# Kernel tuning notes

Measured on AMD Instinct MI355X. Metric: run time of the kernel, lower is better.

## Reference

```python
import jax, jax.numpy as jnp
import numpy as np

B, S, D, H = 8, 1024, 1024, 16
HD = D // H  # head dim 64
NUM_REL = 7


def setup_inputs() -> dict:
    key = jax.random.key(0)
    ks = jax.random.split(key, 10)
    s = 0.02
    return {
        "hidden_states": jax.random.normal(ks[0], (B, S, D), dtype=jnp.float32),
        "attention_mask": jnp.zeros((B, 1, 1, S), dtype=jnp.float32),
        "relation": jax.random.randint(ks[1], (B, S, S), 0, NUM_REL, dtype=jnp.int32),
        "Wq": jax.random.normal(ks[2], (D, D), dtype=jnp.float32) * s,
        "bq": jnp.zeros((D,), dtype=jnp.float32),
        "Wk": jax.random.normal(ks[3], (D, D), dtype=jnp.float32) * s,
        "bk": jnp.zeros((D,), dtype=jnp.float32),
        "Wv": jax.random.normal(ks[4], (D, D), dtype=jnp.float32) * s,
        "bv": jnp.zeros((D,), dtype=jnp.float32),
        "rel_emb": jax.random.normal(ks[5], (NUM_REL, H), dtype=jnp.float32) * s,
    }


def reference(hidden_states, attention_mask, relation, Wq, bq, Wk, bk, Wv, bv, rel_emb):
    def heads(x):  # [B,S,D] -> [B,H,S,HD]
        return x.reshape(B, S, H, HD).transpose(0, 2, 1, 3)

    q = heads(hidden_states @ Wq.T + bq)
    k = heads(hidden_states @ Wk.T + bk)
    v = heads(hidden_states @ Wv.T + bv)

    scores = jnp.einsum("bhqd,bhkd->bhqk", q, k) / jnp.sqrt(jnp.float32(HD))
    # relation bias: gather [B,S,S,H] then move H to dim 1
    rel_bias = rel_emb[relation].transpose(0, 3, 1, 2)  # [B,H,S,S]
    scores = scores + rel_bias + attention_mask
    probs = jax.nn.softmax(scores, axis=-1)  # dropout is identity in eval
    ctx = jnp.einsum("bhqk,bhkd->bhqd", probs, v)
    return ctx.transpose(0, 2, 1, 3).reshape(B, S, D)
```

## Files before the change

### kernel.cpp

```cpp
#include <hip/hip_runtime.h>

#define NB 8
#define NS 1024
#define ND 1024
#define NH 16
#define NHD 64

typedef __attribute__((ext_vector_type(8))) short bf16x8;
typedef __attribute__((ext_vector_type(4))) float f32x4;
typedef __attribute__((ext_vector_type(4))) unsigned int u32x4;

#define GLOAD_LDS16(g, l) __builtin_amdgcn_global_load_lds(                    \
    (const __attribute__((address_space(1))) void*)(g),                        \
    (__attribute__((address_space(3))) void*)(l), 16, 0, 0)

static __device__ __forceinline__ unsigned short f2bf(float f) {
    unsigned int u = __builtin_bit_cast(unsigned int, f);
    unsigned int r = u + 0x7fffu + ((u >> 16) & 1u);
    return (unsigned short)(r >> 16);
}

static __device__ __forceinline__ unsigned int cvtpk(float lo, float hi) {
    unsigned int r;
    asm("v_cvt_pk_bf16_f32 %0, %1, %2" : "=v"(r) : "v"(lo), "v"(hi));
    return r;
}

__global__ void cvt_f32_bf16(const float* __restrict__ in, unsigned short* __restrict__ out, int n) {
    int i = (blockIdx.x * blockDim.x + threadIdx.x) * 4;
    if (i >= n) return;
    float4 v = *reinterpret_cast<const float4*>(in + i);
    ushort4 o;
    o.x = f2bf(v.x); o.y = f2bf(v.y); o.z = f2bf(v.z); o.w = f2bf(v.w);
    *reinterpret_cast<ushort4*>(out + i) = o;
}

__global__ void cvt_w3(const float* __restrict__ Wq, const float* __restrict__ Wk,
                       const float* __restrict__ Wv, unsigned short* __restrict__ out) {
    const float* src = (blockIdx.y == 0) ? Wq : (blockIdx.y == 1) ? Wk : Wv;
    int i = (blockIdx.x * blockDim.x + threadIdx.x) * 4;
    float4 v = *reinterpret_cast<const float4*>(src + i);
    ushort4 o;
    o.x = f2bf(v.x); o.y = f2bf(v.y); o.z = f2bf(v.z); o.w = f2bf(v.w);
    *reinterpret_cast<ushort4*>(out + (size_t)blockIdx.y * (ND * ND) + i) = o;
}

__global__ void pack_rel8(const int* __restrict__ rel, unsigned int* __restrict__ out) {
    int i = blockIdx.x * blockDim.x + threadIdx.x;
    int4 v = reinterpret_cast<const int4*>(rel)[i];
    out[i] = (unsigned)v.x | ((unsigned)v.y << 8) | ((unsigned)v.z << 16) | ((unsigned)v.w << 24);
}

__global__ __launch_bounds__(256) void qkv_gemm(
    const unsigned short* __restrict__ A,
    const unsigned short* __restrict__ Wq, const unsigned short* __restrict__ Wk,
    const unsigned short* __restrict__ Wv,
    const float* __restrict__ bq, const float* __restrict__ bk, const float* __restrict__ bv,
    const float* __restrict__ mask,
    unsigned short* __restrict__ Qo, unsigned short* __restrict__ Ko, unsigned short* __restrict__ Vo)
{
    const int z = blockIdx.z;
    const unsigned short* W = (z == 0) ? Wq : (z == 1) ? Wk : Wv;
    const float* bias = (z == 0) ? bq : (z == 1) ? bk : bv;
    const int m0 = blockIdx.x * 128;
    const int n0 = blockIdx.y * 128;
    const float LOG2E = 1.4426950408889634f;

    __shared__ unsigned short As[128][64];
    __shared__ unsigned short Bs[128][64];

    const int tid = threadIdx.x;
    const int lane = tid & 63;
    const int wave = tid >> 6;
    const int wm = wave >> 1, wn = wave & 1;

    f32x4 acc[4][4] = {};

    const int crow = lane >> 3;
    const int gcol = ((lane & 7) ^ crow) * 8;
    const int kofs = (lane >> 4) * 8;

    for (int kb = 0; kb < ND; kb += 64) {
#pragma unroll
        for (int cc = 0; cc < 4; ++cc) {
            int c = wave * 4 + cc;
            GLOAD_LDS16(&A[(size_t)(m0 + c * 8 + crow) * ND + kb + gcol], &As[c * 8][0]);
            GLOAD_LDS16(&W[(size_t)(n0 + c * 8 + crow) * ND + kb + gcol], &Bs[c * 8][0]);
        }
        __syncthreads();
#pragma unroll
        for (int kk = 0; kk < 2; ++kk) {
            const int colx = (kk * 32 + kofs) ^ ((lane & 7) * 8);
            bf16x8 af[4], bfr[4];
#pragma unroll
            for (int i = 0; i < 4; ++i) {
                af[i]  = *reinterpret_cast<const bf16x8*>(&As[wm * 64 + i * 16 + (lane & 15)][colx]);
                bfr[i] = *reinterpret_cast<const bf16x8*>(&Bs[wn * 64 + i * 16 + (lane & 15)][colx]);
            }
#pragma unroll
            for (int mi = 0; mi < 4; ++mi)
#pragma unroll
                for (int ni = 0; ni < 4; ++ni)
                    acc[mi][ni] = __builtin_amdgcn_mfma_f32_16x16x32_bf16(af[mi], bfr[ni], acc[mi][ni], 0, 0, 0);
        }
        __syncthreads();
    }

#pragma unroll
    for (int ni = 0; ni < 4; ++ni) {
        int n = n0 + wn * 64 + ni * 16 + (lane & 15);
        float bv_ = bias[n];
        int h = n >> 6, hd = n & 63;
#pragma unroll
        for (int mi = 0; mi < 4; ++mi) {
            int m = m0 + wm * 64 + mi * 16 + (lane >> 4) * 4;
            int b = m >> 10, s = m & 1023;
            if (z == 2) {
                float4 mv = *reinterpret_cast<const float4*>(&mask[(size_t)b * NS + s]);
                ushort4 o;
                o.x = f2bf((acc[mi][ni][0] + bv_) * exp2f(mv.x * LOG2E));
                o.y = f2bf((acc[mi][ni][1] + bv_) * exp2f(mv.y * LOG2E));
                o.z = f2bf((acc[mi][ni][2] + bv_) * exp2f(mv.z * LOG2E));
                o.w = f2bf((acc[mi][ni][3] + bv_) * exp2f(mv.w * LOG2E));
                *reinterpret_cast<ushort4*>(&Vo[(((size_t)b * NH + h) * NHD + hd) * NS + s]) = o;
            } else {
                unsigned short* O = (z == 0) ? Qo : Ko;
#pragma unroll
                for (int r2 = 0; r2 < 4; ++r2)
                    O[(((size_t)b * NH + h) * NS + s + r2) * NHD + hd] = f2bf(acc[mi][ni][r2] + bv_);
            }
        }
    }
}

__global__ __launch_bounds__(512) void flash_attn(
    const unsigned short* __restrict__ Q, const unsigned short* __restrict__ Kb,
    const unsigned short* __restrict__ Vt,
    const unsigned char* __restrict__ rel8, const float* __restrict__ rel_emb,
    const float* __restrict__ mask, float* __restrict__ out)
{
    const int q0 = blockIdx.x * 128;
    const int h = blockIdx.y;
    const int b = blockIdx.z;
    const int tid = threadIdx.x, lane = tid & 63, wave = tid >> 6;
    const int g = lane >> 4, l15 = lane & 15;

    __shared__ unsigned short Ks[2][64][64];
    __shared__ unsigned short Vs[2][64][64];
    __shared__ unsigned short s_emask[NS];
    __shared__ float s_re2[8];
    const float LOG2E = 1.4426950408889634f;
    const float SCL2 = 0.125f * 1.4426950408889634f;
    if (tid < 7) s_re2[tid] = rel_emb[tid * NH + h] * LOG2E - 4.0f;

    const unsigned short* Qh = Q  + (((size_t)b * NH + h) * NS) * NHD;
    const unsigned short* Kh = Kb + (((size_t)b * NH + h) * NS) * NHD;
    const unsigned short* Vh = Vt + (((size_t)b * NH + h) * NHD) * NS;
    const int qg = q0 + wave * 16 + l15;
    const unsigned char* __restrict__ relrow = rel8 + (size_t)b * NS * NS + (size_t)qg * NS;
    const float* __restrict__ maskb = mask + (size_t)b * NS;

    bf16x8 qa[2];
    qa[0] = *reinterpret_cast<const bf16x8*>(&Qh[(size_t)qg * NHD + g * 8]);
    qa[1] = *reinterpret_cast<const bf16x8*>(&Qh[(size_t)qg * NHD + 32 + g * 8]);

    f32x4 ctx[4] = {};
    f32x4 l_acc = {};
    float mofs = 0.f;
    bool everscaled = false;

    const int crow = lane >> 3;
    const int gcol = ((lane & 7) ^ crow) * 8;
    const int swz8 = (lane & 7) * 8;

    const int rho = wave * 8 + crow;
    const int kvperm = ((rho >> 5) << 5) + (((rho >> 2) & 3) << 3)
                     + (((rho >> 4) & 1) << 2) + (rho & 3);

#define STAGE(buf, kv)                                                                          \
    {                                                                                           \
        GLOAD_LDS16(&Kh[(size_t)((kv) + kvperm) * NHD + gcol], &Ks[buf][wave * 8][0]);          \
        GLOAD_LDS16(&Vh[(size_t)(wave * 8 + crow) * NS + (kv) + gcol], &Vs[buf][wave * 8][0]);  \
    }

#define LOADRM(S, t0)                                                                \
    {                                                                                \
        r##S##a = *reinterpret_cast<const uint2*>(&relrow[(t0) * 64 + 8 * g]);       \
        r##S##b = *reinterpret_cast<const uint2*>(&relrow[(t0) * 64 + 32 + 8 * g]);  \
    }

    uint2 rAa, rAb, rBa, rBb;

    STAGE(0, 0)
    LOADRM(A, 0)
    s_emask[tid] = f2bf(exp2f(maskb[tid] * LOG2E));
    s_emask[tid + 512] = f2bf(exp2f(maskb[tid + 512] * LOG2E));
    __syncthreads();

#define BODY(cur, S, SN, tc, tn)                                               \
  {                                                                            \
    if ((tn) < 16) {                                                           \
      STAGE(cur ^ 1, (tn) * 64)                                                \
      LOADRM(SN, tn)                                                           \
    }                                                                          \
    f32x4 sc[4] = {};                                                          \
    __builtin_amdgcn_s_setprio(1);                                             \
    _Pragma("unroll")                                                          \
    for (int kk = 0; kk < 2; ++kk) {                                           \
      const int colx = (kk * 32 + g * 8) ^ swz8;                               \
      _Pragma("unroll")                                                        \
      for (int tt = 0; tt < 4; ++tt) {                                         \
        bf16x8 kfrag = *reinterpret_cast<const bf16x8*>(&Ks[cur][tt * 16 + l15][colx]); \
        sc[tt] = __builtin_amdgcn_mfma_f32_16x16x32_bf16(kfrag, qa[kk], sc[tt], 0, 0, 0); \
      }                                                                        \
    }                                                                          \
    __builtin_amdgcn_s_setprio(0);                                             \
    const unsigned int rw[4] = {r##S##a.x, r##S##a.y, r##S##b.x, r##S##b.y};   \
    float pmax = -1e30f;                                                       \
    _Pragma("unroll")                                                          \
    for (int tt = 0; tt < 4; ++tt) {                                           \
      float v0 = fmaf(sc[tt][0], SCL2, s_re2[rw[tt] & 0xFF]);                  \
      float v1 = fmaf(sc[tt][1], SCL2, s_re2[(rw[tt] >> 8) & 0xFF]);           \
      float v2 = fmaf(sc[tt][2], SCL2, s_re2[(rw[tt] >> 16) & 0xFF]);          \
      float v3 = fmaf(sc[tt][3], SCL2, s_re2[rw[tt] >> 24]);                   \
      sc[tt][0] = v0; sc[tt][1] = v1; sc[tt][2] = v2; sc[tt][3] = v3;          \
      pmax = fmaxf(pmax, fmaxf(fmaxf(v0, v1), fmaxf(v2, v3)));                 \
    }                                                                          \
    if (!__all(pmax <= mofs + 8.0f)) {                                         \
      float pm = fmaxf(pmax, __shfl_xor(pmax, 16));                            \
      pm = fmaxf(pm, __shfl_xor(pm, 32));                                      \
      float mnew = fmaxf(mofs, pm);                                            \
      float alpha = exp2f(mofs - mnew);                                        \
      mofs = mnew;                                                             \
      everscaled = true;                                                       \
      float ar[4];                                                             \
      _Pragma("unroll")                                                        \
      for (int r = 0; r < 4; ++r) ar[r] = __shfl(alpha, 4 * g + r);            \
      _Pragma("unroll")                                                        \
      for (int r = 0; r < 4; ++r) l_acc[r] *= ar[r];                           \
      _Pragma("unroll")                                                        \
      for (int ht = 0; ht < 4; ++ht)                                           \
        _Pragma("unroll")                                                      \
        for (int r = 0; r < 4; ++r) ctx[ht][r] *= ar[r];                       \
    }                                                                          \
    unsigned int pw[8];                                                        \
    if (!everscaled) {                                                         \
      _Pragma("unroll")                                                        \
      for (int tt = 0; tt < 4; ++tt) {                                         \
        pw[2 * tt]     = cvtpk(exp2f(sc[tt][0]), exp2f(sc[tt][1]));            \
        pw[2 * tt + 1] = cvtpk(exp2f(sc[tt][2]), exp2f(sc[tt][3]));            \
      }                                                                        \
    } else {                                                                   \
      _Pragma("unroll")                                                        \
      for (int tt = 0; tt < 4; ++tt) {                                         \
        pw[2 * tt]     = cvtpk(exp2f(sc[tt][0] - mofs), exp2f(sc[tt][1] - mofs)); \
        pw[2 * tt + 1] = cvtpk(exp2f(sc[tt][2] - mofs), exp2f(sc[tt][3] - mofs)); \
      }                                                                        \
    }                                                                          \
    __builtin_amdgcn_s_setprio(1);                                             \
    _Pragma("unroll")                                                          \
    for (int kk = 0; kk < 2; ++kk) {                                           \
      u32x4 paw = {pw[4 * kk], pw[4 * kk + 1], pw[4 * kk + 2], pw[4 * kk + 3]};\
      bf16x8 pa = __builtin_bit_cast(bf16x8, paw);                             \
      const int colx = (kk * 32 + g * 8) ^ swz8;                               \
      bf16x8 mfr = *reinterpret_cast<const bf16x8*>(&s_emask[(tc) * 64 + kk * 32 + g * 8]); \
      l_acc = __builtin_amdgcn_mfma_f32_16x16x32_bf16(pa, mfr, l_acc, 0, 0, 0); \
      _Pragma("unroll")                                                        \
      for (int ht = 0; ht < 4; ++ht) {                                         \
        bf16x8 bfrag = *reinterpret_cast<const bf16x8*>(&Vs[cur][ht * 16 + l15][colx]); \
        ctx[ht] = __builtin_amdgcn_mfma_f32_16x16x32_bf16(pa, bfrag, ctx[ht], 0, 0, 0); \
      }                                                                        \
    }                                                                          \
    __builtin_amdgcn_s_setprio(0);                                             \
    __syncthreads();                                                           \
  }

    for (int t = 0; t < 16; t += 2) {
        BODY(0, A, B, t, t + 1)
        BODY(1, B, A, t + 1, t + 2)
    }
#undef BODY
#undef LOADRM
#undef STAGE

    float linv[4];
#pragma unroll
    for (int r = 0; r < 4; ++r) linv[r] = 1.0f / l_acc[r];
#pragma unroll
    for (int ht = 0; ht < 4; ++ht) {
        int hd = ht * 16 + l15;
#pragma unroll
        for (int r = 0; r < 4; ++r) {
            int qo = q0 + wave * 16 + 4 * g + r;
            out[((size_t)b * NS + qo) * ND + h * NHD + hd] = ctx[ht][r] * linv[r];
        }
    }
}

extern "C" void kernel_launch(void* const* d_in, const int* in_sizes, int n_in,
                              void* d_out, int out_size, void* d_ws, size_t ws_size,
                              hipStream_t stream) {
    const float* hs      = (const float*)d_in[0];
    const float* mask    = (const float*)d_in[1];
    const int*   rel     = (const int*)d_in[2];
    const float* Wq      = (const float*)d_in[3];
    const float* bq      = (const float*)d_in[4];
    const float* Wk      = (const float*)d_in[5];
    const float* bk      = (const float*)d_in[6];
    const float* Wv      = (const float*)d_in[7];
    const float* bv      = (const float*)d_in[8];
    const float* rel_emb = (const float*)d_in[9];
    float* out = (float*)d_out;

    char* ws = (char*)d_ws;
    unsigned short* q_bf  = (unsigned short*)(ws);
    unsigned short* k_bf  = (unsigned short*)(ws + ((size_t)16 << 20));
    unsigned short* vt_bf = (unsigned short*)(ws + ((size_t)32 << 20));
    unsigned short* hs_bf = (unsigned short*)(ws + ((size_t)48 << 20));
    unsigned short* w_bf  = (unsigned short*)(ws + ((size_t)64 << 20));
    unsigned char*  rel8  = (unsigned char*)(ws + ((size_t)48 << 20));

    const int nhs = NB * NS * ND;
    const int nw  = ND * ND;
    cvt_f32_bf16<<<nhs / 4 / 256, 256, 0, stream>>>(hs, hs_bf, nhs);
    cvt_w3<<<dim3(nw / 4 / 256, 3), 256, 0, stream>>>(Wq, Wk, Wv, w_bf);

    qkv_gemm<<<dim3((NB * NS) / 128, ND / 128, 3), 256, 0, stream>>>(
        hs_bf, w_bf, w_bf + (size_t)nw, w_bf + (size_t)2 * nw,
        bq, bk, bv, mask, q_bf, k_bf, vt_bf);

    pack_rel8<<<(NB * NS * NS / 4) / 256, 256, 0, stream>>>(rel, (unsigned int*)rel8);

    flash_attn<<<dim3(NS / 128, NH, NB), 512, 0, stream>>>(
        q_bf, k_bf, vt_bf, rel8, rel_emb, mask, out);
}
```

Measured before the change: 169.2 us.

## Fold softmax scale into Q and preload relation bias as MFMA accumulator init

The Q projection epilogue now multiplies by 0.125·log2e, so the attention kernel no longer scales scores. Relation indices are packed pre-shifted by 4 into byte offsets, which avoids an address shift. The bias for the next tile is gathered from LDS at the end of each iteration and used as the initial accumulator of the QK^T MFMAs. This removes the post-MFMA FMA pass and hides the LDS gather latency behind the previous tile, at the cost of 16 more live registers per bias buffer and Q being rounded to bf16 after scaling.

Result: no change. 172.4 us (+1.9%).

```diff
diff --git a/kernel.cpp b/kernel.cpp
--- a/kernel.cpp
+++ b/kernel.cpp
@@ -24,6 +24,10 @@
     unsigned int r;
     asm("v_cvt_pk_bf16_f32 %0, %1, %2" : "=v"(r) : "v"(lo), "v"(hi));
     return r;
+}
+
+static __device__ __forceinline__ float ldre(const float* t, unsigned int byteoff) {
+    return *reinterpret_cast<const float*>(reinterpret_cast<const char*>(t) + byteoff);
 }
 
 __global__ void cvt_f32_bf16(const float* __restrict__ in, unsigned short* __restrict__ out, int n) {
@@ -48,7 +52,8 @@
 __global__ void pack_rel8(const int* __restrict__ rel, unsigned int* __restrict__ out) {
     int i = blockIdx.x * blockDim.x + threadIdx.x;
     int4 v = reinterpret_cast<const int4*>(rel)[i];
-    out[i] = (unsigned)v.x | ((unsigned)v.y << 8) | ((unsigned)v.z << 16) | ((unsigned)v.w << 24);
+    out[i] = ((unsigned)v.x << 2) | ((unsigned)v.y << 10) |
+             ((unsigned)v.z << 18) | ((unsigned)v.w << 26);
 }
 
 __global__ __launch_bounds__(256) void qkv_gemm(
@@ -65,6 +70,7 @@
     const int m0 = blockIdx.x * 128;
     const int n0 = blockIdx.y * 128;
     const float LOG2E = 1.4426950408889634f;
+    const float QSCL = 0.125f * 1.4426950408889634f;
 
     __shared__ unsigned short As[128][64];
     __shared__ unsigned short Bs[128][64];
@@ -123,11 +129,14 @@
                 o.z = f2bf((acc[mi][ni][2] + bv_) * exp2f(mv.z * LOG2E));
                 o.w = f2bf((acc[mi][ni][3] + bv_) * exp2f(mv.w * LOG2E));
                 *reinterpret_cast<ushort4*>(&Vo[(((size_t)b * NH + h) * NHD + hd) * NS + s]) = o;
+            } else if (z == 0) {
+#pragma unroll
+                for (int r2 = 0; r2 < 4; ++r2)
+                    Qo[(((size_t)b * NH + h) * NS + s + r2) * NHD + hd] = f2bf((acc[mi][ni][r2] + bv_) * QSCL);
             } else {
-                unsigned short* O = (z == 0) ? Qo : Ko;
 #pragma unroll
                 for (int r2 = 0; r2 < 4; ++r2)
-                    O[(((size_t)b * NH + h) * NS + s + r2) * NHD + hd] = f2bf(acc[mi][ni][r2] + bv_);
+                    Ko[(((size_t)b * NH + h) * NS + s + r2) * NHD + hd] = f2bf(acc[mi][ni][r2] + bv_);
             }
         }
     }
@@ -150,7 +159,6 @@
     __shared__ unsigned short s_emask[NS];
     __shared__ float s_re2[8];
     const float LOG2E = 1.4426950408889634f;
-    const float SCL2 = 0.125f * 1.4426950408889634f;
     if (tid < 7) s_re2[tid] = rel_emb[tid * NH + h] * LOG2E - 4.0f;
 
     const unsigned short* Qh = Q  + (((size_t)b * NH + h) * NS) * NHD;
@@ -189,13 +197,29 @@
         r##S##b = *reinterpret_cast<const uint2*>(&relrow[(t0) * 64 + 32 + 8 * g]);  \
     }
 
+#define LOADBIAS(S)                                                              \
+    {                                                                            \
+        const unsigned int rw0 = r##S##a.x, rw1 = r##S##a.y;                     \
+        const unsigned int rw2 = r##S##b.x, rw3 = r##S##b.y;                     \
+        b##S[0][0] = ldre(s_re2, rw0 & 0xFF);  b##S[0][1] = ldre(s_re2, (rw0 >> 8) & 0xFF);  \
+        b##S[0][2] = ldre(s_re2, (rw0 >> 16) & 0xFF);  b##S[0][3] = ldre(s_re2, rw0 >> 24);  \
+        b##S[1][0] = ldre(s_re2, rw1 & 0xFF);  b##S[1][1] = ldre(s_re2, (rw1 >> 8) & 0xFF);  \
+        b##S[1][2] = ldre(s_re2, (rw1 >> 16) & 0xFF);  b##S[1][3] = ldre(s_re2, rw1 >> 24);  \
+        b##S[2][0] = ldre(s_re2, rw2 & 0xFF);  b##S[2][1] = ldre(s_re2, (rw2 >> 8) & 0xFF);  \
+        b##S[2][2] = ldre(s_re2, (rw2 >> 16) & 0xFF);  b##S[2][3] = ldre(s_re2, rw2 >> 24);  \
+        b##S[3][0] = ldre(s_re2, rw3 & 0xFF);  b##S[3][1] = ldre(s_re2, (rw3 >> 8) & 0xFF);  \
+        b##S[3][2] = ldre(s_re2, (rw3 >> 16) & 0xFF);  b##S[3][3] = ldre(s_re2, rw3 >> 24);  \
+    }
+
     uint2 rAa, rAb, rBa, rBb;
+    f32x4 bA[4], bB[4];
 
     STAGE(0, 0)
     LOADRM(A, 0)
     s_emask[tid] = f2bf(exp2f(maskb[tid] * LOG2E));
     s_emask[tid + 512] = f2bf(exp2f(maskb[tid + 512] * LOG2E));
     __syncthreads();
+    LOADBIAS(A)
 
 #define BODY(cur, S, SN, tc, tn)                                               \
   {                                                                            \
@@ -203,7 +227,9 @@
       STAGE(cur ^ 1, (tn) * 64)                                                \
       LOADRM(SN, tn)                                                           \
     }                                                                          \
-    f32x4 sc[4] = {};                                                          \
+    f32x4 sc[4];                                                               \
+    _Pragma("unroll")                                                          \
+    for (int tt = 0; tt < 4; ++tt) sc[tt] = b##S[tt];       \
     __builtin_amdgcn_s_setprio(1);                                             \
     _Pragma("unroll")                                                          \
     for (int kk = 0; kk < 2; ++kk) {                                           \
@@ -215,17 +241,11 @@
       }                                                                        \
     }                                                                          \
     __builtin_amdgcn_s_setprio(0);                                             \
-    const unsigned int rw[4] = {r##S##a.x, r##S##a.y, r##S##b.x, r##S##b.y};   \
     float pmax = -1e30f;                                                       \
     _Pragma("unroll")                                                          \
-    for (int tt = 0; tt < 4; ++tt) {                                           \
-      float v0 = fmaf(sc[tt][0], SCL2, s_re2[rw[tt] & 0xFF]);                  \
-      float v1 = fmaf(sc[tt][1], SCL2, s_re2[(rw[tt] >> 8) & 0xFF]);           \
-      float v2 = fmaf(sc[tt][2], SCL2, s_re2[(rw[tt] >> 16) & 0xFF]);          \
-      float v3 = fmaf(sc[tt][3], SCL2, s_re2[rw[tt] >> 24]);                   \
-      sc[tt][0] = v0; sc[tt][1] = v1; sc[tt][2] = v2; sc[tt][3] = v3;          \
-      pmax = fmaxf(pmax, fmaxf(fmaxf(v0, v1), fmaxf(v2, v3)));                 \
-    }                                                                          \
+    for (int tt = 0; tt < 4; ++tt)                                             \
+      pmax = fmaxf(pmax, fmaxf(fmaxf(sc[tt][0], sc[tt][1]),                    \
+                               fmaxf(sc[tt][2], sc[tt][3])));                  \
     if (!__all(pmax <= mofs + 8.0f)) {                                         \
       float pm = fmaxf(pmax, __shfl_xor(pmax, 16));                            \
       pm = fmaxf(pm, __shfl_xor(pm, 32));                                      \
@@ -272,6 +292,7 @@
       }                                                                        \
     }                                                                          \
     __builtin_amdgcn_s_setprio(0);                                             \
+    if ((tn) < 16) LOADBIAS(SN)    \
     __syncthreads();                                                           \
   }
 
@@ -280,6 +301,7 @@
         BODY(1, B, A, t + 1, t + 2)
     }
 #undef BODY
+#undef LOADBIAS
 #undef LOADRM
 #undef STAGE
 
```
